# Kernel optimization log

Measured on AMD Instinct MI355X. Metric: run time of the kernel, lower is better.

Reference implementation:

```python
import jax, jax.numpy as jnp
import numpy as np

HID = 256   # hiddenDims
QD = 64     # queryDims
B = 16      # number of segments
LQ = 2048   # query tokens per segment
LH = 2048   # key/value tokens per segment
EPS = 1e-5


def _layer_norm(x, w, b):
    m = jnp.mean(x, axis=-1, keepdims=True)
    v = jnp.mean((x - m) ** 2, axis=-1, keepdims=True)
    return (x - m) / jnp.sqrt(v + EPS) * w + b


def setup_inputs() -> dict:
    key = jax.random.key(0)
    ks = jax.random.split(key, 8)
    q = jax.random.normal(ks[0], (B * LQ, HID), jnp.float32)
    h = jax.random.normal(ks[1], (B * LH, HID), jnp.float32)
    s = 1.0 / np.sqrt(HID)
    WQ = jax.random.normal(ks[2], (QD, HID), jnp.float32) * s
    WK = jax.random.normal(ks[3], (QD, HID), jnp.float32) * s
    WV = jax.random.normal(ks[4], (HID, HID), jnp.float32) * s
    fc_w = jax.random.normal(ks[5], (HID, HID), jnp.float32) * s
    fc_b = jax.random.normal(ks[6], (HID,), jnp.float32) * 0.01
    norm0_w = jnp.ones((HID,), jnp.float32)
    norm0_b = jnp.zeros((HID,), jnp.float32)
    norm1_w = jnp.ones((HID,), jnp.float32)
    norm1_b = jnp.zeros((HID,), jnp.float32)
    qlens = jnp.full((B,), LQ, jnp.int32)
    hlens = jnp.full((B,), LH, jnp.int32)
    return {"q": q, "h": h, "WQ": WQ, "WK": WK, "WV": WV,
            "fc_w": fc_w, "fc_b": fc_b,
            "norm0_w": norm0_w, "norm0_b": norm0_b,
            "norm1_w": norm1_w, "norm1_b": norm1_b,
            "qlens": qlens, "hlens": hlens}


def reference(q, h, WQ, WK, WV, fc_w, fc_b,
              norm0_w, norm0_b, norm1_w, norm1_b, qlens, hlens):
    # segments are equal-length, so the ragged per-segment loop is exactly
    # batched block-diagonal attention over [B, L, D] views.
    nb = qlens.shape[0]
    Lq = q.shape[0] // nb
    Lh = h.shape[0] // hlens.shape[0]
    D = q.shape[-1]
    qq = (q @ WQ.T).reshape(nb, Lq, -1)          # [B, Lq, QD]
    k = (h @ WK.T).reshape(nb, Lh, -1)           # [B, Lh, QD]
    v = (h @ WV.T).reshape(nb, Lh, D)            # [B, Lh, D]
    scale = 1.0 / jnp.sqrt(jnp.asarray(qq.shape[-1], jnp.float32))
    a = jax.nn.softmax(jnp.einsum('bqc,bkc->bqk', qq, k) * scale, axis=-1)
    att = jnp.einsum('bqk,bkd->bqd', a, v).reshape(-1, D)  # concat of segments
    x = _layer_norm(q + att, norm0_w, norm0_b)
    hres = x @ fc_w.T + fc_b
    return _layer_norm(x + jax.nn.relu(hres), norm1_w, norm1_b)
```

## Files before the change

### kernel.cpp

```cpp
#include <hip/hip_runtime.h>
#include <hip/hip_bf16.h>

#define HID 256
#define QD 64
#define NSEG 16
#define SLQ 2048
#define SLH 2048


typedef __attribute__((ext_vector_type(8))) short bf16x8;
typedef __attribute__((ext_vector_type(8))) __bf16 bf16x8b;
typedef __attribute__((ext_vector_type(4))) float f32x4;
typedef __attribute__((ext_vector_type(4))) short s16x4;

#define BAR_LDS() asm volatile("s_waitcnt lgkmcnt(0)\n\ts_barrier" ::: "memory")

static __device__ __forceinline__ f32x4 mfma16(bf16x8 a, bf16x8 b, f32x4 c) {
  return __builtin_amdgcn_mfma_f32_16x16x32_bf16(
      __builtin_bit_cast(bf16x8b, a), __builtin_bit_cast(bf16x8b, b), c, 0, 0, 0);
}

static __device__ __forceinline__ short f2bf(float x) {
  union { float f; unsigned u; } v; v.f = x;
  unsigned r = v.u + 0x7fffu + ((v.u >> 16) & 1u);
  return (short)(r >> 16);
}

static __device__ __forceinline__ float bf2f(short s) {
  union { unsigned u; float f; } v;
  v.u = ((unsigned)(unsigned short)s) << 16;
  return v.f;
}

static __device__ __forceinline__ void pack_w(const float* __restrict__ s,
                                              short* __restrict__ d, int i) {
  int j = i & 7, l16 = (i >> 3) & 15, quad = (i >> 7) & 3, ks = (i >> 9) & 7,
      n = i >> 12;
  d[i] = f2bf(s[(size_t)(n * 16 + l16) * HID + ks * 32 + quad * 8 + j]);
}

static __device__ __forceinline__ void grid_barrier(unsigned* cnt,
                                                    unsigned* flag,
                                                    unsigned nblk) {
  __syncthreads();
  if (threadIdx.x == 0) {
    __threadfence();
    unsigned old = atomicAdd(cnt, 1u);
    if (old == nblk - 1u) {
      atomicExch(flag, 1u);
    } else {
      while (atomicAdd(flag, 0u) == 0u) __builtin_amdgcn_s_sleep(2);
    }
    __threadfence();
  }
  __syncthreads();
}

__global__ __launch_bounds__(512, 4) void fused_kernel(
    const float* __restrict__ q, const float* __restrict__ h,
    const float* __restrict__ WQ, const float* __restrict__ WK,
    const float* __restrict__ WV, const float* __restrict__ fcw,
    const float* __restrict__ fcb, const float* __restrict__ n0w,
    const float* __restrict__ n0b, const float* __restrict__ n1w,
    const float* __restrict__ n1b, short* __restrict__ wqb,
    short* __restrict__ wkb, short* __restrict__ wvb,
    short* __restrict__ fwb, short* __restrict__ kb,
    short* __restrict__ vt, unsigned* __restrict__ bar,
    float* __restrict__ out) {
  __shared__ short p_lds[2][64][136];
  __shared__ short qx[4096];
  __shared__ float plsum[4][2][16];
  __shared__ float rs[2][2][64];

  int wave = threadIdx.x >> 6, lane = threadIdx.x & 63;
  int quad = lane >> 4, l16 = lane & 15;
  int b = blockIdx.x;

  {
    int gi = b * 512 + threadIdx.x;
    if (gi < 16384) pack_w(WQ, wqb, gi);
    else if (gi < 32768) pack_w(WK, wkb, gi - 16384);
    else if (gi < 98304) pack_w(WV, wvb, gi - 32768);
    else if (gi < 163840) pack_w(fcw, fwb, gi - 98304);
  }
  grid_barrier(bar + 0, bar + 16, 512u);

  {
    short (*hb)[264] = (short(*)[264]) & p_lds[0][0][0];
    int m0 = b * 64;
#pragma unroll
    for (int i = 0; i < 8; ++i) {
      int idx = i * 512 + threadIdx.x;
      int row = idx >> 6, col = (idx & 63) * 4;
      f32x4 v = *(const f32x4*)(h + (size_t)(m0 + row) * HID + col);
      s16x4 pk;
#pragma unroll
      for (int j = 0; j < 4; ++j) pk[j] = f2bf(v[j]);
      *(s16x4*)&hb[row][col] = pk;
    }
    __syncthreads();
    int mw = (wave & 3) * 16;
    int mtb = (wave >> 2) * 8;
    f32x4 kacc[4];
    f32x4 vacc[8];
#pragma unroll
    for (int n = 0; n < 4; ++n) kacc[n] = f32x4{0.f, 0.f, 0.f, 0.f};
#pragma unroll
    for (int n = 0; n < 8; ++n) vacc[n] = f32x4{0.f, 0.f, 0.f, 0.f};
#pragma unroll
    for (int ks = 0; ks < 8; ++ks) {
      bf16x8 a = *(const bf16x8*)&hb[mw + l16][ks * 32 + quad * 8];
      if (wave < 4) {
#pragma unroll
        for (int n = 0; n < 4; ++n) {
          bf16x8 wb = *(const bf16x8*)(wkb + (size_t)((n * 8 + ks) * 64 + lane) * 8);
          kacc[n] = mfma16(a, wb, kacc[n]);
        }
      }
#pragma unroll
      for (int mt = 0; mt < 8; ++mt) {
        bf16x8 wf = *(const bf16x8*)(wvb + (size_t)(((mtb + mt) * 8 + ks) * 64 + lane) * 8);
        vacc[mt] = mfma16(wf, a, vacc[mt]);
      }
    }
    __syncthreads();
    if (wave < 4) {
      char* kx = (char*)&hb[mw][0];
#pragma unroll
      for (int n = 0; n < 4; ++n)
#pragma unroll
        for (int r = 0; r < 4; ++r) {
          int k16 = quad * 4 + r;
          int bo = (k16 * 128 + (n * 16 + l16) * 2) ^ ((k16 & 7) << 4);
          *(short*)(kx + bo) = f2bf(kacc[n][r]);
        }
      asm volatile("s_waitcnt lgkmcnt(0)" ::: "memory");
      int seg = (m0 + mw) >> 11;
      int g = ((m0 + mw) & 2047) >> 4;
      short* kdst = kb + (size_t)seg * 131072 + (size_t)g * 1024 + lane * 8;
#pragma unroll
      for (int p = 0; p < 2; ++p) {
        int bo = (l16 * 128 + p * 64 + quad * 16) ^ ((l16 & 7) << 4);
        *(bf16x8*)(kdst + p * 512) = *(bf16x8*)(kx + bo);
      }
    }
    __syncthreads();
    {
      char* vbuf = (char*)&hb[0][0];
#pragma unroll
      for (int mt = 0; mt < 8; ++mt)
#pragma unroll
        for (int r = 0; r < 4; ++r) {
          int dv = (mtb + mt) * 16 + quad * 4 + r;
          int bo = (dv * 128 + (mw + l16) * 2) ^ ((dv & 7) << 4);
          *(short*)(vbuf + bo) = f2bf(vacc[mt][r]);
        }
      __syncthreads();
      int seg = m0 >> 11;
      int t0 = m0 & 2047;
      int kt = t0 >> 7;
      int ksb = (t0 >> 5) & 3;
      short* vdst = vt + (size_t)seg * 524288;
#pragma unroll
      for (int i = 0; i < 4; ++i) {
        int u = wave * 4 + i;
        int ksl = u >> 4, d16 = u & 15;
        int dim = d16 * 16 + l16;
        int bo = (dim * 128 + ksl * 64 + quad * 16) ^ ((dim & 7) << 4);
        size_t unit = (size_t)((kt * 4 + ksb + ksl) * 16 + d16);
        *(bf16x8*)(vdst + unit * 512 + lane * 8) = *(bf16x8*)(vbuf + bo);
      }
    }
  }
  grid_barrier(bar + 32, bar + 48, 512u);

  int qg = wave >> 1, kh = wave & 1;
  int xcd = b & 7, li = b >> 3;
  int seg = xcd * 2 + (li >> 5);
  int tile = li & 31;
  int qrow0 = seg * SLQ + tile * 64;
  const short* kseg = kb + (size_t)seg * 131072;
  const short* vseg = vt + (size_t)seg * 524288;

  const float cexp = 0.125f * 1.44269504f;
  bf16x8 kpre[4][2];

#define LOADK(KT)                                                               \
  {                                                                             \
    _Pragma("unroll") for (int t = 0; t < 4; ++t) {                             \
      const short* kp = kseg + (size_t)((KT) * 8 + kh * 4 + t) * 1024 + lane * 8;\
      kpre[t][0] = *(const bf16x8*)kp;                                          \
      kpre[t][1] = *(const bf16x8*)(kp + 512);                                  \
    }                                                                           \
  }

  LOADK(tile & 15)

  short (*st)[264] = (short(*)[264]) & p_lds[0][0][0];
  bf16x8 qf0, qf1;
  {
    const float* qsrc = q + (size_t)qrow0 * HID;
#pragma unroll
    for (int i = 0; i < 8; ++i) {
      int idx = i * 512 + threadIdx.x;
      int row = idx >> 6, col = (idx & 63) * 4;
      f32x4 v = *(const f32x4*)(qsrc + (size_t)row * HID + col);
      s16x4 pk;
#pragma unroll
      for (int j = 0; j < 4; ++j) pk[j] = f2bf(v[j]);
      *(s16x4*)&st[row][col] = pk;
    }
    __syncthreads();
    f32x4 qacc[2];
    qacc[0] = f32x4{0.f, 0.f, 0.f, 0.f};
    qacc[1] = f32x4{0.f, 0.f, 0.f, 0.f};
#pragma unroll
    for (int ks = 0; ks < 8; ++ks) {
      bf16x8 a = *(const bf16x8*)&st[qg * 16 + l16][ks * 32 + quad * 8];
#pragma unroll
      for (int ni = 0; ni < 2; ++ni) {
        int n = kh * 2 + ni;
        bf16x8 wb = *(const bf16x8*)(wqb + (size_t)((n * 8 + ks) * 64 + lane) * 8);
        qacc[ni] = mfma16(a, wb, qacc[ni]);
      }
    }
    BAR_LDS();
#pragma unroll
    for (int ni = 0; ni < 2; ++ni)
#pragma unroll
      for (int r = 0; r < 4; ++r) {
        int n = kh * 2 + ni;
        int colp = (n & 1) * 16 + l16;
        qx[(qg * 2 + (n >> 1)) * 512 + ((colp >> 3) * 16 + quad * 4 + r) * 8 +
           (colp & 7)] = f2bf(qacc[ni][r]);
      }
    BAR_LDS();
    const short* qxp = qx + qg * 1024 + lane * 8;
    qf0 = *(const bf16x8*)qxp;
    qf1 = *(const bf16x8*)(qxp + 512);
  }

  f32x4 o[4][2];
#pragma unroll
  for (int m = 0; m < 4; ++m)
#pragma unroll
    for (int n = 0; n < 2; ++n) o[m][n] = f32x4{0.f, 0.f, 0.f, 0.f};
  float lsum = 0.f;

#define S_PHASE(BUF)                                                            \
  {                                                                             \
    f32x4 s[4];                                                                 \
    _Pragma("unroll") for (int t = 0; t < 4; ++t) {                             \
      f32x4 a = f32x4{0.f, 0.f, 0.f, 0.f};                                      \
      a = mfma16(kpre[t][0], qf0, a);                                           \
      a = mfma16(kpre[t][1], qf1, a);                                           \
      s[t] = a;                                                                 \
    }                                                                           \
    _Pragma("unroll") for (int t = 0; t < 4; ++t) {                             \
      float p0 = __builtin_amdgcn_exp2f(s[t][0] * cexp);                        \
      float p1 = __builtin_amdgcn_exp2f(s[t][1] * cexp);                        \
      float p2 = __builtin_amdgcn_exp2f(s[t][2] * cexp);                        \
      float p3 = __builtin_amdgcn_exp2f(s[t][3] * cexp);                        \
      lsum += (p0 + p1) + (p2 + p3);                                            \
      s16x4 pk;                                                                 \
      pk[0] = f2bf(p0); pk[1] = f2bf(p1); pk[2] = f2bf(p2); pk[3] = f2bf(p3);   \
      *(s16x4*)&p_lds[BUF][qg * 16 + l16][kh * 64 + t * 16 + quad * 4] = pk;    \
    }                                                                           \
  }

#define PV_PHASE(KT, BUF)                                                       \
  {                                                                             \
    _Pragma("unroll") for (int ks = 0; ks < 4; ++ks) {                          \
      bf16x8 pf[4];                                                             \
      _Pragma("unroll") for (int m = 0; m < 4; ++m)                             \
        pf[m] = *(const bf16x8*)&p_lds[BUF][m * 16 + l16][ks * 32 + quad * 8];  \
      _Pragma("unroll") for (int n = 0; n < 2; ++n) {                           \
        const short* vp = vseg +                                                \
            ((size_t)((KT) * 4 + ks) * 16 + wave * 2 + n) * 512 + lane * 8;     \
        bf16x8 vf = *(const bf16x8*)vp;                                         \
        _Pragma("unroll") for (int m = 0; m < 4; ++m)                           \
          o[m][n] = mfma16(pf[m], vf, o[m][n]);                                 \
      }                                                                         \
    }                                                                           \
  }

  S_PHASE(0)
  LOADK((tile + 1) & 15)
  BAR_LDS();
#pragma unroll 1
  for (int j = 1; j < 16; ++j) {
    S_PHASE(j & 1)
    if (j < 15) LOADK((tile + j + 1) & 15)
    PV_PHASE((tile + j - 1) & 15, (j - 1) & 1)
    BAR_LDS();
  }
  PV_PHASE((tile + 15) & 15, 1)

  lsum += __shfl_xor(lsum, 16);
  lsum += __shfl_xor(lsum, 32);

  BAR_LDS();
  if (lane < 16) plsum[qg][kh][lane] = lsum;
  short (*ob)[264] = (short(*)[264]) & p_lds[0][0][0];
#pragma unroll
  for (int m = 0; m < 4; ++m)
#pragma unroll
    for (int n = 0; n < 2; ++n)
#pragma unroll
      for (int r = 0; r < 4; ++r)
        ob[m * 16 + quad * 4 + r][wave * 32 + n * 16 + l16] = f2bf(o[m][n][r]);
  BAR_LDS();

  {
    int row = wave * 8 + (lane >> 3);
    int c0 = (lane & 7) * 32;
    float linv = 1.f / (plsum[row >> 4][0][row & 15] + plsum[row >> 4][1][row & 15]);
    float y[32];
    float s1 = 0.f, s2 = 0.f;
    const float* qp = q + (size_t)(qrow0 + row) * HID + c0;
#pragma unroll
    for (int k = 0; k < 4; ++k) {
      bf16x8 ov = *(const bf16x8*)&ob[row][c0 + k * 8];
      f32x4 qa = *(const f32x4*)(qp + k * 8);
      f32x4 qb = *(const f32x4*)(qp + k * 8 + 4);
#pragma unroll
      for (int j = 0; j < 4; ++j) {
        float yv = qa[j] + bf2f(ov[j]) * linv;
        y[k * 8 + j] = yv;
        s1 += yv; s2 += yv * yv;
      }
#pragma unroll
      for (int j = 0; j < 4; ++j) {
        float yv = qb[j] + bf2f(ov[4 + j]) * linv;
        y[k * 8 + 4 + j] = yv;
        s1 += yv; s2 += yv * yv;
      }
    }
    s1 += __shfl_xor(s1, 1); s2 += __shfl_xor(s2, 1);
    s1 += __shfl_xor(s1, 2); s2 += __shfl_xor(s2, 2);
    s1 += __shfl_xor(s1, 4); s2 += __shfl_xor(s2, 4);
    float mean = s1 * (1.f / HID);
    float var = s2 * (1.f / HID) - mean * mean;
    float rstd = rsqrtf(var + 1e-5f);
#pragma unroll
    for (int k = 0; k < 4; ++k) {
      f32x4 wa = *(const f32x4*)(n0w + c0 + k * 8);
      f32x4 wb = *(const f32x4*)(n0w + c0 + k * 8 + 4);
      f32x4 ba = *(const f32x4*)(n0b + c0 + k * 8);
      f32x4 bb = *(const f32x4*)(n0b + c0 + k * 8 + 4);
      s16x4 o0, o1;
#pragma unroll
      for (int j = 0; j < 4; ++j) {
        o0[j] = f2bf((y[k * 8 + j] - mean) * rstd * wa[j] + ba[j]);
        o1[j] = f2bf((y[k * 8 + 4 + j] - mean) * rstd * wb[j] + bb[j]);
      }
      *(s16x4*)&ob[row][c0 + k * 8] = o0;
      *(s16x4*)&ob[row][c0 + k * 8 + 4] = o1;
    }
  }
  BAR_LDS();

  {
    f32x4 facc[8];
#pragma unroll
    for (int n2 = 0; n2 < 8; ++n2) facc[n2] = f32x4{0.f, 0.f, 0.f, 0.f};
#pragma unroll
    for (int ks = 0; ks < 8; ++ks) {
      bf16x8 a = *(const bf16x8*)&ob[qg * 16 + l16][ks * 32 + quad * 8];
#pragma unroll
      for (int n2 = 0; n2 < 8; ++n2) {
        int n = kh * 8 + n2;
        bf16x8 wb = *(const bf16x8*)(fwb + (size_t)((n * 8 + ks) * 64 + lane) * 8);
        facc[n2] = mfma16(a, wb, facc[n2]);
      }
    }
#pragma unroll
    for (int r = 0; r < 4; ++r) {
      int row = qg * 16 + quad * 4 + r;
      float s = 0.f, s2 = 0.f;
#pragma unroll
      for (int n2 = 0; n2 < 8; ++n2) {
        int col = kh * 128 + n2 * 16 + l16;
        float hres = fmaxf(facc[n2][r] + fcb[col], 0.f);
        float yv = bf2f(ob[row][col]) + hres;
        s += yv; s2 += yv * yv;
      }
      s += __shfl_xor(s, 1); s2 += __shfl_xor(s2, 1);
      s += __shfl_xor(s, 2); s2 += __shfl_xor(s2, 2);
      s += __shfl_xor(s, 4); s2 += __shfl_xor(s2, 4);
      s += __shfl_xor(s, 8); s2 += __shfl_xor(s2, 8);
      if (l16 == 0) { rs[0][kh][row] = s; rs[1][kh][row] = s2; }
    }
    BAR_LDS();
#pragma unroll
    for (int r = 0; r < 4; ++r) {
      int row = qg * 16 + quad * 4 + r;
      float st1 = rs[0][0][row] + rs[0][1][row];
      float st2 = rs[1][0][row] + rs[1][1][row];
      float mean = st1 * (1.f / HID);
      float var = st2 * (1.f / HID) - mean * mean;
      float rstd = rsqrtf(var + 1e-5f);
      float* op = out + (size_t)(qrow0 + row) * HID;
#pragma unroll
      for (int n2 = 0; n2 < 8; ++n2) {
        int col = kh * 128 + n2 * 16 + l16;
        float hres = fmaxf(facc[n2][r] + fcb[col], 0.f);
        float yv = bf2f(ob[row][col]) + hres;
        op[col] = (yv - mean) * rstd * n1w[col] + n1b[col];
      }
    }
  }
#undef LOADK
#undef S_PHASE
#undef PV_PHASE
}

extern "C" void kernel_launch(void* const* d_in, const int* in_sizes, int n_in,
                              void* d_out, int out_size, void* d_ws, size_t ws_size,
                              hipStream_t stream) {
  const float* q = (const float*)d_in[0];
  const float* h = (const float*)d_in[1];
  const float* WQ = (const float*)d_in[2];
  const float* WK = (const float*)d_in[3];
  const float* WV = (const float*)d_in[4];
  const float* fc_w = (const float*)d_in[5];
  const float* fc_b = (const float*)d_in[6];
  const float* n0w = (const float*)d_in[7];
  const float* n0b = (const float*)d_in[8];
  const float* n1w = (const float*)d_in[9];
  const float* n1b = (const float*)d_in[10];

  char* ws = (char*)d_ws;
  short* kb = (short*)(ws);
  short* vt = (short*)(ws + ((size_t)4 << 20));
  short* wqb = (short*)(ws + ((size_t)20 << 20));
  short* wkb = (short*)(ws + ((size_t)20 << 20) + 32 * 1024);
  short* wvb = (short*)(ws + ((size_t)20 << 20) + 64 * 1024);
  short* fwb = (short*)(ws + ((size_t)20 << 20) + 192 * 1024);
  unsigned* bar = (unsigned*)(ws + ((size_t)21 << 20));

  hipMemsetAsync(bar, 0, 256, stream);
  fused_kernel<<<512, 512, 0, stream>>>(q, h, WQ, WK, WV, fc_w, fc_b,
                                        n0w, n0b, n1w, n1b, wqb, wkb, wvb,
                                        fwb, kb, vt, bar, (float*)d_out);
}
```

Measured before the change: 286.1 us.

## Split weight cast into separate kernel and use per-segment barriers

Weight packing to bf16 moves out of the fused kernel into its own small launch, which removes the first grid-wide barrier. The second grid barrier becomes a per-segment counter, and each block's K/V projection rows are remapped to its own segment. Each block signals after writing its K/V and then computes its Q projection before waiting, so that work overlaps the wait. The cost is an extra kernel launch, in exchange for narrower, partly hidden synchronisation.

```diff
diff --git a/kernel.cpp b/kernel.cpp
--- a/kernel.cpp
+++ b/kernel.cpp
@@ -39,32 +39,27 @@
   d[i] = f2bf(s[(size_t)(n * 16 + l16) * HID + ks * 32 + quad * 8 + j]);
 }
 
-static __device__ __forceinline__ void grid_barrier(unsigned* cnt,
-                                                    unsigned* flag,
-                                                    unsigned nblk) {
-  __syncthreads();
-  if (threadIdx.x == 0) {
-    __threadfence();
-    unsigned old = atomicAdd(cnt, 1u);
-    if (old == nblk - 1u) {
-      atomicExch(flag, 1u);
-    } else {
-      while (atomicAdd(flag, 0u) == 0u) __builtin_amdgcn_s_sleep(2);
-    }
-    __threadfence();
-  }
-  __syncthreads();
-}
-
-__global__ __launch_bounds__(512, 4) void fused_kernel(
+__global__ __launch_bounds__(256) void cast4_kernel(const float* __restrict__ s0, short* __restrict__ d0, int n0,
+                                                    const float* __restrict__ s1, short* __restrict__ d1, int n1,
+                                                    const float* __restrict__ s2, short* __restrict__ d2, int n2,
+                                                    const float* __restrict__ s3, short* __restrict__ d3, int n3) {
+  int i = blockIdx.x * 256 + threadIdx.x;
+  if (i < n0) pack_w(s0, d0, i);
+  int j = i - n0;
+  if (j >= 0 && j < n1) pack_w(s1, d1, j);
+  int k = j - n1;
+  if (k >= 0 && k < n2) pack_w(s2, d2, k);
+  int l = k - n2;
+  if (l >= 0 && l < n3) pack_w(s3, d3, l);
+}
+
+__global__ __launch_bounds__(512, 4) void attn_kernel(
     const float* __restrict__ q, const float* __restrict__ h,
-    const float* __restrict__ WQ, const float* __restrict__ WK,
-    const float* __restrict__ WV, const float* __restrict__ fcw,
+    const short* __restrict__ wqb, const short* __restrict__ wkb,
+    const short* __restrict__ wvb, const short* __restrict__ fwb,
     const float* __restrict__ fcb, const float* __restrict__ n0w,
     const float* __restrict__ n0b, const float* __restrict__ n1w,
-    const float* __restrict__ n1b, short* __restrict__ wqb,
-    short* __restrict__ wkb, short* __restrict__ wvb,
-    short* __restrict__ fwb, short* __restrict__ kb,
+    const float* __restrict__ n1b, short* __restrict__ kb,
     short* __restrict__ vt, unsigned* __restrict__ bar,
     float* __restrict__ out) {
   __shared__ short p_lds[2][64][136];
@@ -75,19 +70,14 @@
   int wave = threadIdx.x >> 6, lane = threadIdx.x & 63;
   int quad = lane >> 4, l16 = lane & 15;
   int b = blockIdx.x;
-
-  {
-    int gi = b * 512 + threadIdx.x;
-    if (gi < 16384) pack_w(WQ, wqb, gi);
-    else if (gi < 32768) pack_w(WK, wkb, gi - 16384);
-    else if (gi < 98304) pack_w(WV, wvb, gi - 32768);
-    else if (gi < 163840) pack_w(fcw, fwb, gi - 98304);
-  }
-  grid_barrier(bar + 0, bar + 16, 512u);
+  int xcd = b & 7, li = b >> 3;
+  int seg = xcd * 2 + (li >> 5);
+  int tile = li & 31;
+  int qrow0 = seg * SLQ + tile * 64;
 
   {
     short (*hb)[264] = (short(*)[264]) & p_lds[0][0][0];
-    int m0 = b * 64;
+    int m0 = seg * SLH + tile * 64;
 #pragma unroll
     for (int i = 0; i < 8; ++i) {
       int idx = i * 512 + threadIdx.x;
@@ -135,8 +125,7 @@
           *(short*)(kx + bo) = f2bf(kacc[n][r]);
         }
       asm volatile("s_waitcnt lgkmcnt(0)" ::: "memory");
-      int seg = (m0 + mw) >> 11;
-      int g = ((m0 + mw) & 2047) >> 4;
+      int g = (tile * 64 + mw) >> 4;
       short* kdst = kb + (size_t)seg * 131072 + (size_t)g * 1024 + lane * 8;
 #pragma unroll
       for (int p = 0; p < 2; ++p) {
@@ -156,8 +145,7 @@
           *(short*)(vbuf + bo) = f2bf(vacc[mt][r]);
         }
       __syncthreads();
-      int seg = m0 >> 11;
-      int t0 = m0 & 2047;
+      int t0 = tile * 64;
       int kt = t0 >> 7;
       int ksb = (t0 >> 5) & 3;
       short* vdst = vt + (size_t)seg * 524288;
@@ -172,16 +160,66 @@
       }
     }
   }
-  grid_barrier(bar + 32, bar + 48, 512u);
+
+  __syncthreads();
+  if (threadIdx.x == 0) {
+    __threadfence();
+    atomicAdd(&bar[seg * 32], 1u);
+  }
 
   int qg = wave >> 1, kh = wave & 1;
-  int xcd = b & 7, li = b >> 3;
-  int seg = xcd * 2 + (li >> 5);
-  int tile = li & 31;
-  int qrow0 = seg * SLQ + tile * 64;
+  short (*st)[264] = (short(*)[264]) & p_lds[0][0][0];
+  bf16x8 qf0, qf1;
+  {
+    const float* qsrc = q + (size_t)qrow0 * HID;
+#pragma unroll
+    for (int i = 0; i < 8; ++i) {
+      int idx = i * 512 + threadIdx.x;
+      int row = idx >> 6, col = (idx & 63) * 4;
+      f32x4 v = *(const f32x4*)(qsrc + (size_t)row * HID + col);
+      s16x4 pk;
+#pragma unroll
+      for (int j = 0; j < 4; ++j) pk[j] = f2bf(v[j]);
+      *(s16x4*)&st[row][col] = pk;
+    }
+    __syncthreads();
+    f32x4 qacc[2];
+    qacc[0] = f32x4{0.f, 0.f, 0.f, 0.f};
+    qacc[1] = f32x4{0.f, 0.f, 0.f, 0.f};
+#pragma unroll
+    for (int ks = 0; ks < 8; ++ks) {
+      bf16x8 a = *(const bf16x8*)&st[qg * 16 + l16][ks * 32 + quad * 8];
+#pragma unroll
+      for (int ni = 0; ni < 2; ++ni) {
+        int n = kh * 2 + ni;
+        bf16x8 wb = *(const bf16x8*)(wqb + (size_t)((n * 8 + ks) * 64 + lane) * 8);
+        qacc[ni] = mfma16(a, wb, qacc[ni]);
+      }
+    }
+    BAR_LDS();
+#pragma unroll
+    for (int ni = 0; ni < 2; ++ni)
+#pragma unroll
+      for (int r = 0; r < 4; ++r) {
+        int n = kh * 2 + ni;
+        int colp = (n & 1) * 16 + l16;
+        qx[(qg * 2 + (n >> 1)) * 512 + ((colp >> 3) * 16 + quad * 4 + r) * 8 +
+           (colp & 7)] = f2bf(qacc[ni][r]);
+      }
+    BAR_LDS();
+    const short* qxp = qx + qg * 1024 + lane * 8;
+    qf0 = *(const bf16x8*)qxp;
+    qf1 = *(const bf16x8*)(qxp + 512);
+  }
+
+  if (threadIdx.x == 0) {
+    while (atomicAdd(&bar[seg * 32], 0u) < 32u) __builtin_amdgcn_s_sleep(2);
+    __threadfence();
+  }
+  __syncthreads();
+
   const short* kseg = kb + (size_t)seg * 131072;
   const short* vseg = vt + (size_t)seg * 524288;
-
   const float cexp = 0.125f * 1.44269504f;
   bf16x8 kpre[4][2];
 
@@ -192,52 +230,6 @@
       kpre[t][0] = *(const bf16x8*)kp;                                          \
       kpre[t][1] = *(const bf16x8*)(kp + 512);                                  \
     }                                                                           \
-  }
-
-  LOADK(tile & 15)
-
-  short (*st)[264] = (short(*)[264]) & p_lds[0][0][0];
-  bf16x8 qf0, qf1;
-  {
-    const float* qsrc = q + (size_t)qrow0 * HID;
-#pragma unroll
-    for (int i = 0; i < 8; ++i) {
-      int idx = i * 512 + threadIdx.x;
-      int row = idx >> 6, col = (idx & 63) * 4;
-      f32x4 v = *(const f32x4*)(qsrc + (size_t)row * HID + col);
-      s16x4 pk;
-#pragma unroll
-      for (int j = 0; j < 4; ++j) pk[j] = f2bf(v[j]);
-      *(s16x4*)&st[row][col] = pk;
-    }
-    __syncthreads();
-    f32x4 qacc[2];
-    qacc[0] = f32x4{0.f, 0.f, 0.f, 0.f};
-    qacc[1] = f32x4{0.f, 0.f, 0.f, 0.f};
-#pragma unroll
-    for (int ks = 0; ks < 8; ++ks) {
-      bf16x8 a = *(const bf16x8*)&st[qg * 16 + l16][ks * 32 + quad * 8];
-#pragma unroll
-      for (int ni = 0; ni < 2; ++ni) {
-        int n = kh * 2 + ni;
-        bf16x8 wb = *(const bf16x8*)(wqb + (size_t)((n * 8 + ks) * 64 + lane) * 8);
-        qacc[ni] = mfma16(a, wb, qacc[ni]);
-      }
-    }
-    BAR_LDS();
-#pragma unroll
-    for (int ni = 0; ni < 2; ++ni)
-#pragma unroll
-      for (int r = 0; r < 4; ++r) {
-        int n = kh * 2 + ni;
-        int colp = (n & 1) * 16 + l16;
-        qx[(qg * 2 + (n >> 1)) * 512 + ((colp >> 3) * 16 + quad * 4 + r) * 8 +
-           (colp & 7)] = f2bf(qacc[ni][r]);
-      }
-    BAR_LDS();
-    const short* qxp = qx + qg * 1024 + lane * 8;
-    qf0 = *(const bf16x8*)qxp;
-    qf1 = *(const bf16x8*)(qxp + 512);
   }
 
   f32x4 o[4][2];
@@ -284,6 +276,7 @@
     }                                                                           \
   }
 
+  LOADK(tile & 15)
   S_PHASE(0)
   LOADK((tile + 1) & 15)
   BAR_LDS();
@@ -439,8 +432,10 @@
   short* fwb = (short*)(ws + ((size_t)20 << 20) + 192 * 1024);
   unsigned* bar = (unsigned*)(ws + ((size_t)21 << 20));
 
-  hipMemsetAsync(bar, 0, 256, stream);
-  fused_kernel<<<512, 512, 0, stream>>>(q, h, WQ, WK, WV, fc_w, fc_b,
-                                        n0w, n0b, n1w, n1b, wqb, wkb, wvb,
-                                        fwb, kb, vt, bar, (float*)d_out);
-}
+  hipMemsetAsync(bar, 0, 16 * 32 * sizeof(unsigned), stream);
+  cast4_kernel<<<640, 256, 0, stream>>>(WQ, wqb, QD * HID, WK, wkb, QD * HID,
+                                        WV, wvb, HID * HID, fc_w, fwb, HID * HID);
+  attn_kernel<<<512, 512, 0, stream>>>(q, h, wqb, wkb, wvb, fwb, fc_b,
+                                       n0w, n0b, n1w, n1b, kb, vt, bar,
+                                       (float*)d_out);
+}
```

Result: faster. 252.8 us (-11.6%).
